# Kernel optimization log

Measured on AMD Instinct MI355X. Metric: run time of the kernel, lower is better.

## Reference

```python
import jax, jax.numpy as jnp
import numpy as np

H = 1024      # hidden_size
NH = 16       # num_attention_heads
HD = H // NH  # attention_head_size = 64
B, S = 2, 2048


def setup_inputs() -> dict:
    key = jax.random.key(0)
    ks = jax.random.split(key, 8)
    scale = 1.0 / np.sqrt(H)
    return {
        "hidden_states": jax.random.normal(ks[0], (B, S, H), dtype=jnp.float32),
        "attention_mask": jnp.zeros((B, 1, 1, S), dtype=jnp.float32),
        "Wq": jax.random.normal(ks[1], (H, H), dtype=jnp.float32) * scale,
        "bq": jax.random.normal(ks[2], (H,), dtype=jnp.float32) * 0.02,
        "Wk": jax.random.normal(ks[3], (H, H), dtype=jnp.float32) * scale,
        "bk": jax.random.normal(ks[4], (H,), dtype=jnp.float32) * 0.02,
        "Wv": jax.random.normal(ks[5], (H, H), dtype=jnp.float32) * scale,
        "bv": jax.random.normal(ks[6], (H,), dtype=jnp.float32) * 0.02,
    }


def _split_heads(x):
    # [B,S,H] -> [B,NH,S,HD]
    b, s, _ = x.shape
    return x.reshape(b, s, NH, HD).transpose(0, 2, 1, 3)


def reference(hidden_states, attention_mask, Wq, bq, Wk, bk, Wv, bv):
    q = _split_heads(hidden_states @ Wq.T + bq)  # [B,NH,S,HD]
    k = _split_heads(hidden_states @ Wk.T + bk)
    v = _split_heads(hidden_states @ Wv.T + bv)
    scores = jnp.einsum("bhqd,bhkd->bhqk", q, k) / np.sqrt(HD).astype(np.float32)
    scores = scores + attention_mask  # additive mask, broadcast over heads/queries
    weights = jax.nn.softmax(scores, axis=-1)  # dropout is identity in eval mode
    ctx = jnp.einsum("bhqk,bhkd->bhqd", weights, v)  # [B,NH,S,HD]
    return ctx.transpose(0, 2, 1, 3).reshape(hidden_states.shape[0], hidden_states.shape[1], H)
```

## Files before the change

kernel.cpp:

```cpp
#include <hip/hip_runtime.h>
#include <hip/hip_bf16.h>
#include <math.h>

#define HSZ   1024
#define NHEAD 16
#define HDIM  64
#define BATCH 2
#define SEQ   2048

#define LOG2E 1.4426950408889634f

typedef __attribute__((ext_vector_type(8))) short short8;
typedef __attribute__((ext_vector_type(4))) short short4_t;
typedef __attribute__((ext_vector_type(4))) float floatx4;

typedef __attribute__((address_space(1))) const unsigned int gu32;
typedef __attribute__((address_space(3))) unsigned int lu32;

__device__ __forceinline__ void g2lds16(const void* g, void* l) {
    __builtin_amdgcn_global_load_lds((gu32*)g, (lu32*)l, 16, 0, 0);
}

__device__ __forceinline__ short f2bf(float f) {
    union { float f; unsigned u; } v; v.f = f;
    unsigned r = (v.u + 0x7FFF + ((v.u >> 16) & 1)) >> 16;
    return (short)r;
}

__device__ __forceinline__ unsigned pk2(float a, float b) {
    __hip_bfloat162 h = __float22bfloat162_rn(make_float2(a, b));
    return *(unsigned*)&h;
}

__device__ __forceinline__ float ex2(float x) {
#if __has_builtin(__builtin_amdgcn_exp2f)
    return __builtin_amdgcn_exp2f(x);
#else
    return exp2f(x);
#endif
}

__global__ __launch_bounds__(256) void convert_kernel(
    const float4* __restrict__ X, const float4* __restrict__ Wq,
    const float4* __restrict__ Wk, const float4* __restrict__ Wv,
    const float4* __restrict__ Mask,
    short4_t* __restrict__ Xb, short4_t* __restrict__ Wb,
    float4* __restrict__ Mw)
{
    int idx = blockIdx.x * 256 + threadIdx.x;
    if (idx >= 1835008) {
        int t = idx - 1835008;
        float4 f = Mask[t];
        float4 o;
        o.x = f.x * LOG2E; o.y = f.y * LOG2E;
        o.z = f.z * LOG2E; o.w = f.w * LOG2E;
        Mw[t] = o;
        return;
    }
    const float4* src; short4_t* dst;
    if (idx < 1048576) { src = X + idx; dst = Xb + idx; }
    else {
        int t = idx - 1048576;
        int sel = t >> 18;
        int wi  = t & 0x3FFFF;
        src = (sel == 0 ? Wq : sel == 1 ? Wk : Wv) + wi;
        dst = Wb + (sel << 18) + wi;
    }
    float4 f = *src;
    short4_t o;
    o.x = f2bf(f.x); o.y = f2bf(f.y); o.z = f2bf(f.z); o.w = f2bf(f.w);
    *dst = o;
}

__global__ __launch_bounds__(256, 3) void qkv_mfma_kernel(
    const short* __restrict__ Xb, const short* __restrict__ Wb,
    const float* __restrict__ bq, const float* __restrict__ bk,
    const float* __restrict__ bv,
    short* __restrict__ qo, short* __restrict__ ko, short* __restrict__ vT)
{
    __shared__ short Sm[128 * 132];
    short* As = Sm;
    short* Bs = Sm + 8192;

    const int tid  = threadIdx.x;
    const int lane = tid & 63;
    const int w    = tid >> 6;
    const int l    = lane & 15, quad = lane >> 4;
    const int gM   = blockIdx.y * 128;
    const int gN   = blockIdx.x * 128;
    const int wm   = (w >> 1) * 64, wn = (w & 1) * 64;
    const int ci   = lane >> 3, pb = lane & 7;

    floatx4 acc[4][4] = {};

    for (int kt = 0; kt < HSZ / 64; ++kt) {
        const int k0 = kt * 64;
        __syncthreads();
        #pragma unroll
        for (int u = 0; u < 4; ++u) {
            int c  = w * 4 + u;
            int r  = c * 8 + ci;
            int lb = pb ^ (r & 7);
            g2lds16(Xb + (size_t)(gM + r) * HSZ + k0 + lb * 8, &As[c * 512]);
            g2lds16(Wb + (size_t)(gN + r) * HSZ + k0 + lb * 8, &Bs[c * 512]);
        }
        __syncthreads();
        #pragma unroll
        for (int kk = 0; kk < 2; ++kk) {
            short8 a[4], b[4];
            #pragma unroll
            for (int i = 0; i < 4; ++i) {
                int m = wm + i * 16 + l;
                a[i] = *(const short8*)&As[m * 64 + (((quad + kk * 4) ^ (m & 7)) << 3)];
                int n = wn + i * 16 + l;
                b[i] = *(const short8*)&Bs[n * 64 + (((quad + kk * 4) ^ (n & 7)) << 3)];
            }
            #pragma unroll
            for (int i = 0; i < 4; ++i)
                #pragma unroll
                for (int j = 0; j < 4; ++j)
                    acc[i][j] = __builtin_amdgcn_mfma_f32_16x16x32_bf16(
                        a[i], b[j], acc[i][j], 0, 0, 0);
        }
    }

    const int mat = gN >> 10;

    if (mat == 2) {
        __syncthreads();
        #pragma unroll
        for (int j = 0; j < 4; ++j) {
            int fl = wn + j * 16 + l;
            float bv_ = bv[(gN & 1023) + fl];
            #pragma unroll
            for (int i = 0; i < 4; ++i)
                #pragma unroll
                for (int r = 0; r < 4; ++r)
                    Sm[fl * 132 + wm + i * 16 + quad * 4 + r]
                        = f2bf(acc[i][j][r] + bv_);
        }
        __syncthreads();
        const int bb = gM >> 11, ss0 = gM & (SEQ - 1);
        #pragma unroll
        for (int it = 0; it < 16; ++it) {
            int f = (tid >> 5) + it * 8;
            int c = (tid & 31) * 4;
            short4_t val = *(const short4_t*)&Sm[f * 132 + c];
            int b = (c >> 2) & 15;
            int cp = (c & ~63) | ((((b & 8) | ((b & 3) << 1) | ((b >> 2) & 1))) << 2);
            int nft = (gN & 1023) + f;
            int head = nft >> 6, d = nft & 63;
            *(short4_t*)&vT[(((size_t)(bb * NHEAD + head)) * HDIM + d) * SEQ
                            + ss0 + cp] = val;
        }
        return;
    }

    const float* bias = (mat == 0) ? bq : bk;
    short* dst        = (mat == 0) ? qo : ko;
    const float qscale = (mat == 0) ? 0.125f * LOG2E : 1.0f;

    #pragma unroll
    for (int j = 0; j < 4; ++j) {
        int nft = (gN & 1023) + wn + j * 16 + l;
        float bv_ = bias[nft];
        int head = nft >> 6, d = nft & 63;
        #pragma unroll
        for (int i = 0; i < 4; ++i) {
            #pragma unroll
            for (int r = 0; r < 4; ++r) {
                int gr = gM + wm + i * 16 + quad * 4 + r;
                int bb = gr >> 11, ss = gr & (SEQ - 1);
                float val = (acc[i][j][r] + bv_) * qscale;
                dst[((((size_t)bb * NHEAD + head) * SEQ + ss) << 6) + d] = f2bf(val);
            }
        }
    }
}

__global__ __launch_bounds__(512, 4) void attn_kernel(
    const short* __restrict__ Qg, const short* __restrict__ Kg,
    const short* __restrict__ VTg, const float* __restrict__ maskw,
    float* __restrict__ out)
{
    __shared__ short Qs[128 * 64];
    __shared__ alignas(16) short Kb3[3][64 * 64];
    __shared__ alignas(16) short Vb3[3][64 * 64];
    __shared__ alignas(16) float Mf[SEQ];

    const int tid  = threadIdx.x;
    const int lane = tid & 63;
    const int w    = tid >> 6;
    const int l    = lane & 15, quad = lane >> 4;
    const int idx  = blockIdx.x;
    const int bh   = idx & 31;
    const int qt   = idx >> 5;
    const int batch = bh >> 4, head = bh & 15;
    const int ci = lane >> 3, pb = lane & 7;

    const short* Qb = Qg + ((size_t)bh * SEQ + qt * 128) * HDIM;
    const short* Kg_ = Kg + (size_t)bh * SEQ * HDIM;
    const short* Vg_ = VTg + (size_t)bh * HDIM * SEQ;
    const float* mrow = maskw + (size_t)batch * SEQ;

    #pragma unroll
    for (int u = 0; u < 2; ++u) {
        int c = w * 2 + u;
        int r = c * 8 + ci;
        int lb = pb ^ (r & 7);
        g2lds16(Qb + (size_t)r * HDIM + lb * 8, &Qs[c * 512]);
    }
    g2lds16(mrow + w * 256 + lane * 4, &Mf[w * 256]);
    {
        int r = w * 8 + ci;
        int lb = pb ^ (r & 7);
        g2lds16(Kg_ + (size_t)r * HDIM + lb * 8,          &Kb3[0][w * 512]);
        g2lds16(Kg_ + (size_t)(64 + r) * HDIM + lb * 8,   &Kb3[1][w * 512]);
        g2lds16(Kg_ + (size_t)(128 + r) * HDIM + lb * 8,  &Kb3[2][w * 512]);
        g2lds16(Vg_ + (size_t)r * SEQ + lb * 8,           &Vb3[0][w * 512]);
        g2lds16(Vg_ + (size_t)r * SEQ + 64 + lb * 8,      &Vb3[1][w * 512]);
    }
    __syncthreads();

    short8 aq[2];
    #pragma unroll
    for (int kk = 0; kk < 2; ++kk) {
        int m = w * 16 + l;
        aq[kk] = *(const short8*)&Qs[m * 64 + (((quad + kk * 4) ^ (m & 7)) << 3)];
    }

    const short8 bones = {(short)0x3F80, (short)0x3F80, (short)0x3F80, (short)0x3F80,
                          (short)0x3F80, (short)0x3F80, (short)0x3F80, (short)0x3F80};

    floatx4 o[4] = {};
    floatx4 ol = {0.f, 0.f, 0.f, 0.f};
    floatx4 sA[4], sB[4];

    const short* kR; const short* kP; short* kW;
    const short* vR; const short* vP; short* vW;

    auto DMAK = [&](int t) {
        int r = w * 8 + ci;
        int lb = pb ^ (r & 7);
        g2lds16(Kg_ + (size_t)(t * 64 + r) * HDIM + lb * 8, kW + w * 512);
    };
    auto DMAV = [&](int t) {
        int r = w * 8 + ci;
        int lb = pb ^ (r & 7);
        g2lds16(Vg_ + (size_t)r * SEQ + t * 64 + lb * 8, vW + w * 512);
    };
    auto ROT = [&]() {
        const short* tk = kR; kR = kP; kP = kW; kW = (short*)tk;
        const short* tv = vR; vR = vP; vP = vW; vW = (short*)tv;
    };

    auto QKT = [&](floatx4 (&s)[4], const short* kbuf, int u1) {
        const float* mg = &Mf[u1 * 64];
        #pragma unroll
        for (int m = 0; m < 4; ++m) {
            float4 mq = *(const float4*)&mg[m * 16 + quad * 4];
            floatx4 ini = {mq.x, mq.y, mq.z, mq.w};
            s[m] = ini;
        }
        #pragma unroll
        for (int kk = 0; kk < 2; ++kk) {
            short8 ak[4];
            #pragma unroll
            for (int m = 0; m < 4; ++m) {
                int kr = m * 16 + l;
                ak[m] = *(const short8*)&kbuf[kr * 64 + (((quad + kk * 4) ^ (kr & 7)) << 3)];
            }
            __builtin_amdgcn_s_setprio(1);
            #pragma unroll
            for (int m = 0; m < 4; ++m)
                s[m] = __builtin_amdgcn_mfma_f32_16x16x32_bf16(
                    ak[m], aq[kk], s[m], 0, 0, 0);
            __builtin_amdgcn_s_setprio(0);
        }
    };

    auto SMPV = [&](floatx4 (&s)[4], const short* vbuf) {
        #pragma unroll
        for (int m = 0; m < 4; ++m) {
            s[m][0] = ex2(s[m][0]);
            s[m][1] = ex2(s[m][1]);
            s[m][2] = ex2(s[m][2]);
            s[m][3] = ex2(s[m][3]);
        }
        #pragma unroll
        for (int kb = 0; kb < 2; ++kb) {
            short8 bvf[4];
            #pragma unroll
            for (int nd = 0; nd < 4; ++nd) {
                int d = nd * 16 + l;
                bvf[nd] = *(const short8*)&vbuf[d * 64 + (((kb * 4 + quad) ^ (d & 7)) << 3)];
            }
            short8 ap;
            {
                union { unsigned u[4]; short8 s8; } pu;
                pu.u[0] = pk2(s[2 * kb][0], s[2 * kb][1]);
                pu.u[1] = pk2(s[2 * kb][2], s[2 * kb][3]);
                pu.u[2] = pk2(s[2 * kb + 1][0], s[2 * kb + 1][1]);
                pu.u[3] = pk2(s[2 * kb + 1][2], s[2 * kb + 1][3]);
                ap = pu.s8;
            }
            __builtin_amdgcn_s_setprio(1);
            #pragma unroll
            for (int nd = 0; nd < 4; ++nd)
                o[nd] = __builtin_amdgcn_mfma_f32_16x16x32_bf16(
                    ap, bvf[nd], o[nd], 0, 0, 0);
            ol = __builtin_amdgcn_mfma_f32_16x16x32_bf16(
                ap, bones, ol, 0, 0, 0);
            __builtin_amdgcn_s_setprio(0);
        }
    };

    QKT(sA, &Kb3[0][0], 0);
    __syncthreads();
    kR = &Kb3[1][0]; kP = &Kb3[2][0]; kW = &Kb3[0][0];
    vR = &Vb3[0][0]; vP = &Vb3[1][0]; vW = &Vb3[2][0];

#define PHASE_BAR(N)                                        \
    asm volatile("s_waitcnt vmcnt(" #N ")" ::: "memory");   \
    __builtin_amdgcn_s_barrier();                           \
    asm volatile("" ::: "memory");

    for (int t = 0; t < 28; t += 2) {
        DMAK(t + 3); DMAV(t + 2);
        QKT(sB, kR, t + 1);
        SMPV(sA, vR);
        PHASE_BAR(2)
        ROT();
        DMAK(t + 4); DMAV(t + 3);
        QKT(sA, kR, t + 2);
        SMPV(sB, vR);
        PHASE_BAR(2)
        ROT();
    }
    DMAK(31); DMAV(30);
    QKT(sB, kR, 29);
    SMPV(sA, vR);
    PHASE_BAR(2)
    ROT();
    DMAV(31);
    QKT(sA, kR, 30);
    SMPV(sB, vR);
    PHASE_BAR(1)
    ROT();
    QKT(sB, kR, 31);
    SMPV(sA, vR);
    PHASE_BAR(0)
    ROT();
    SMPV(sB, vR);
#undef PHASE_BAR

    #pragma unroll
    for (int r = 0; r < 4; ++r) {
        float inv = 1.0f / ol[r];
        int qrow = qt * 128 + w * 16 + quad * 4 + r;
        #pragma unroll
        for (int nd = 0; nd < 4; ++nd)
            out[((size_t)batch * SEQ + qrow) * HSZ + head * HDIM + nd * 16 + l]
                = o[nd][r] * inv;
    }
}

extern "C" void kernel_launch(void* const* d_in, const int* in_sizes, int n_in,
                              void* d_out, int out_size, void* d_ws, size_t ws_size,
                              hipStream_t stream) {
    const float* hs   = (const float*)d_in[0];
    const float* mask = (const float*)d_in[1];
    const float* Wq   = (const float*)d_in[2];
    const float* bq   = (const float*)d_in[3];
    const float* Wk   = (const float*)d_in[4];
    const float* bk   = (const float*)d_in[5];
    const float* Wv   = (const float*)d_in[6];
    const float* bv   = (const float*)d_in[7];
    float* out = (float*)d_out;

    short* Xb = (short*)d_ws;
    short* Wb = Xb + 4194304;
    short* qb = Wb + 3145728;
    short* kb = qb + 4194304;
    short* vT = kb + 4194304;
    float* Mw = (float*)(vT + 4194304);

    convert_kernel<<<7172, 256, 0, stream>>>(
        (const float4*)hs, (const float4*)Wq, (const float4*)Wk, (const float4*)Wv,
        (const float4*)mask, (short4_t*)Xb, (short4_t*)Wb, (float4*)Mw);

    dim3 g2(3 * HSZ / 128, BATCH * SEQ / 128);
    qkv_mfma_kernel<<<g2, 256, 0, stream>>>(Xb, Wb, bq, bk, bv, qb, kb, vT);

    attn_kernel<<<512, 512, 0, stream>>>(qb, kb, vT, Mw, out);
}
```

Measured before the change: 156.5 us.

## Load Q fragments directly from global and fold mask scaling into attention

Drops the Q staging buffer in LDS and loads each wave's Q MFMA fragments straight from global memory into registers. Removes the mask pre-scaling pass from the convert kernel and instead multiplies the raw mask by log2(e) when initializing score accumulators. This frees 16KB of LDS per block, which may allow more resident blocks, and removes a small extra write and read of the scaled mask. In exchange the Q reads are less coalesced, and a few extra multiplies land in the inner loop.

```diff
diff --git a/kernel.cpp b/kernel.cpp
--- a/kernel.cpp
+++ b/kernel.cpp
@@ -43,20 +43,9 @@
 __global__ __launch_bounds__(256) void convert_kernel(
     const float4* __restrict__ X, const float4* __restrict__ Wq,
     const float4* __restrict__ Wk, const float4* __restrict__ Wv,
-    const float4* __restrict__ Mask,
-    short4_t* __restrict__ Xb, short4_t* __restrict__ Wb,
-    float4* __restrict__ Mw)
+    short4_t* __restrict__ Xb, short4_t* __restrict__ Wb)
 {
     int idx = blockIdx.x * 256 + threadIdx.x;
-    if (idx >= 1835008) {
-        int t = idx - 1835008;
-        float4 f = Mask[t];
-        float4 o;
-        o.x = f.x * LOG2E; o.y = f.y * LOG2E;
-        o.z = f.z * LOG2E; o.w = f.w * LOG2E;
-        Mw[t] = o;
-        return;
-    }
     const float4* src; short4_t* dst;
     if (idx < 1048576) { src = X + idx; dst = Xb + idx; }
     else {
@@ -183,7 +172,6 @@
     const short* __restrict__ VTg, const float* __restrict__ maskw,
     float* __restrict__ out)
 {
-    __shared__ short Qs[128 * 64];
     __shared__ alignas(16) short Kb3[3][64 * 64];
     __shared__ alignas(16) short Vb3[3][64 * 64];
     __shared__ alignas(16) float Mf[SEQ];
@@ -203,13 +191,6 @@
     const short* Vg_ = VTg + (size_t)bh * HDIM * SEQ;
     const float* mrow = maskw + (size_t)batch * SEQ;
 
-    #pragma unroll
-    for (int u = 0; u < 2; ++u) {
-        int c = w * 2 + u;
-        int r = c * 8 + ci;
-        int lb = pb ^ (r & 7);
-        g2lds16(Qb + (size_t)r * HDIM + lb * 8, &Qs[c * 512]);
-    }
     g2lds16(mrow + w * 256 + lane * 4, &Mf[w * 256]);
     {
         int r = w * 8 + ci;
@@ -220,14 +201,13 @@
         g2lds16(Vg_ + (size_t)r * SEQ + lb * 8,           &Vb3[0][w * 512]);
         g2lds16(Vg_ + (size_t)r * SEQ + 64 + lb * 8,      &Vb3[1][w * 512]);
     }
-    __syncthreads();
 
     short8 aq[2];
     #pragma unroll
-    for (int kk = 0; kk < 2; ++kk) {
-        int m = w * 16 + l;
-        aq[kk] = *(const short8*)&Qs[m * 64 + (((quad + kk * 4) ^ (m & 7)) << 3)];
-    }
+    for (int kk = 0; kk < 2; ++kk)
+        aq[kk] = *(const short8*)&Qb[(w * 16 + l) * HDIM + kk * 32 + quad * 8];
+
+    __syncthreads();
 
     const short8 bones = {(short)0x3F80, (short)0x3F80, (short)0x3F80, (short)0x3F80,
                           (short)0x3F80, (short)0x3F80, (short)0x3F80, (short)0x3F80};
@@ -259,7 +239,8 @@
         #pragma unroll
         for (int m = 0; m < 4; ++m) {
             float4 mq = *(const float4*)&mg[m * 16 + quad * 4];
-            floatx4 ini = {mq.x, mq.y, mq.z, mq.w};
+            floatx4 ini = {mq.x * LOG2E, mq.y * LOG2E,
+                           mq.z * LOG2E, mq.w * LOG2E};
             s[m] = ini;
         }
         #pragma unroll
@@ -383,14 +364,13 @@
     short* qb = Wb + 3145728;
     short* kb = qb + 4194304;
     short* vT = kb + 4194304;
-    float* Mw = (float*)(vT + 4194304);
-
-    convert_kernel<<<7172, 256, 0, stream>>>(
+
+    convert_kernel<<<7168, 256, 0, stream>>>(
         (const float4*)hs, (const float4*)Wq, (const float4*)Wk, (const float4*)Wv,
-        (const float4*)mask, (short4_t*)Xb, (short4_t*)Wb, (float4*)Mw);
+        (short4_t*)Xb, (short4_t*)Wb);
 
     dim3 g2(3 * HSZ / 128, BATCH * SEQ / 128);
     qkv_mfma_kernel<<<g2, 256, 0, stream>>>(Xb, Wb, bq, bk, bv, qb, kb, vT);
 
-    attn_kernel<<<512, 512, 0, stream>>>(qb, kb, vT, Mw, out);
-}
+    attn_kernel<<<512, 512, 0, stream>>>(qb, kb, vT, mask, out);
+}
```

Measured after the change: 158.5 us. About the same (+1.3%).

## Rework QKV GEMM into 256x256 tiles with double-buffered async LDS pipeline

Applied to the files above, without the earlier changes.

The QKV projection GEMM now uses 256x256 output tiles per 512-thread block, giving 192 blocks instead of 768. K-tiles are double-buffered in LDS, and the next tile's global-to-LDS loads are interleaved with the four MFMA phases, using explicit barriers and s_setprio around the MFMA bursts. The intent is to hide global load latency and raise data reuse per block, at the cost of more LDS and registers per block. The V transpose epilogue is split into two halves so it fits the reused LDS buffer.

```diff
diff --git a/kernel.cpp b/kernel.cpp
--- a/kernel.cpp
+++ b/kernel.cpp
@@ -72,86 +72,118 @@
     *dst = o;
 }
 
-__global__ __launch_bounds__(256, 3) void qkv_mfma_kernel(
+__global__ __launch_bounds__(512, 2) void qkv_mfma_kernel(
     const short* __restrict__ Xb, const short* __restrict__ Wb,
     const float* __restrict__ bq, const float* __restrict__ bk,
     const float* __restrict__ bv,
     short* __restrict__ qo, short* __restrict__ ko, short* __restrict__ vT)
 {
-    __shared__ short Sm[128 * 132];
-    short* As = Sm;
-    short* Bs = Sm + 8192;
+    __shared__ alignas(16) short As[2][2][128 * 64];
+    __shared__ alignas(16) short Bs[2][2][128 * 64];
 
     const int tid  = threadIdx.x;
     const int lane = tid & 63;
     const int w    = tid >> 6;
     const int l    = lane & 15, quad = lane >> 4;
-    const int gM   = blockIdx.y * 128;
-    const int gN   = blockIdx.x * 128;
-    const int wm   = (w >> 1) * 64, wn = (w & 1) * 64;
+    const int wr   = w >> 2, wc = w & 3;
     const int ci   = lane >> 3, pb = lane & 7;
-
-    floatx4 acc[4][4] = {};
-
-    for (int kt = 0; kt < HSZ / 64; ++kt) {
-        const int k0 = kt * 64;
-        __syncthreads();
-        #pragma unroll
-        for (int u = 0; u < 4; ++u) {
-            int c  = w * 4 + u;
+    const int bid  = blockIdx.x;
+    const int gM   = (bid / 12) * 256;
+    const int gN   = (bid % 12) * 256;
+
+    auto STAGE = [&](int t, int db, int op , int half) {
+        #pragma unroll
+        for (int u = 0; u < 2; ++u) {
+            int c  = w * 2 + u;
             int r  = c * 8 + ci;
             int lb = pb ^ (r & 7);
-            g2lds16(Xb + (size_t)(gM + r) * HSZ + k0 + lb * 8, &As[c * 512]);
-            g2lds16(Wb + (size_t)(gN + r) * HSZ + k0 + lb * 8, &Bs[c * 512]);
-        }
-        __syncthreads();
-        #pragma unroll
-        for (int kk = 0; kk < 2; ++kk) {
+            const short* src = (op == 0)
+                ? Xb + (size_t)(gM + half * 128 + r) * HSZ + t * 64 + lb * 8
+                : Wb + (size_t)(gN + half * 128 + r) * HSZ + t * 64 + lb * 8;
+            short* dst = (op == 0 ? &As[db][half][0] : &Bs[db][half][0]) + c * 512;
+            g2lds16(src, dst);
+        }
+    };
+
+    floatx4 acc[8][4] = {};
+
+    STAGE(0, 0, 0, 0); STAGE(0, 0, 0, 1);
+    STAGE(0, 0, 1, 0); STAGE(0, 0, 1, 1);
+    asm volatile("s_waitcnt vmcnt(0)" ::: "memory");
+    __builtin_amdgcn_s_barrier();
+
+    for (int t = 0; t < HSZ / 64; ++t) {
+        const int d = t & 1, dn = d ^ 1;
+        const short* Ah = &As[d][wr][0];
+        const short* Bh = &Bs[d][wc >> 1][0];
+        const int bbase = (wc & 1) * 64;
+        const bool more = (t + 1 < HSZ / 64);
+        #pragma unroll
+        for (int ph = 0; ph < 4; ++ph) {
+            const int mh = ph & 1, kkv = ph >> 1;
             short8 a[4], b[4];
             #pragma unroll
             for (int i = 0; i < 4; ++i) {
-                int m = wm + i * 16 + l;
-                a[i] = *(const short8*)&As[m * 64 + (((quad + kk * 4) ^ (m & 7)) << 3)];
-                int n = wn + i * 16 + l;
-                b[i] = *(const short8*)&Bs[n * 64 + (((quad + kk * 4) ^ (n & 7)) << 3)];
-            }
+                int lr = (mh * 4 + i) * 16 + l;
+                a[i] = *(const short8*)&Ah[lr * 64 + (((quad + kkv * 4) ^ (lr & 7)) << 3)];
+                int br = bbase + i * 16 + l;
+                b[i] = *(const short8*)&Bh[br * 64 + (((quad + kkv * 4) ^ (br & 7)) << 3)];
+            }
+            if (more) {
+                if      (ph == 0) STAGE(t + 1, dn, 0, 0);
+                else if (ph == 1) STAGE(t + 1, dn, 1, 0);
+                else if (ph == 2) STAGE(t + 1, dn, 1, 1);
+                else              STAGE(t + 1, dn, 0, 1);
+            }
+            __builtin_amdgcn_s_barrier();
+            asm volatile("s_waitcnt lgkmcnt(0)" ::: "memory");
+            __builtin_amdgcn_s_setprio(1);
             #pragma unroll
             for (int i = 0; i < 4; ++i)
                 #pragma unroll
                 for (int j = 0; j < 4; ++j)
-                    acc[i][j] = __builtin_amdgcn_mfma_f32_16x16x32_bf16(
-                        a[i], b[j], acc[i][j], 0, 0, 0);
+                    acc[mh * 4 + i][j] = __builtin_amdgcn_mfma_f32_16x16x32_bf16(
+                        a[i], b[j], acc[mh * 4 + i][j], 0, 0, 0);
+            __builtin_amdgcn_s_setprio(0);
+            if (ph == 3) asm volatile("s_waitcnt vmcnt(0)" ::: "memory");
+            __builtin_amdgcn_s_barrier();
         }
     }
 
     const int mat = gN >> 10;
 
     if (mat == 2) {
-        __syncthreads();
-        #pragma unroll
-        for (int j = 0; j < 4; ++j) {
-            int fl = wn + j * 16 + l;
-            float bv_ = bv[(gN & 1023) + fl];
-            #pragma unroll
-            for (int i = 0; i < 4; ++i)
+        short* Smv = &As[0][0][0];
+        const int bb = gM >> 11, ss0 = gM & (SEQ - 1);
+        #pragma unroll
+        for (int h = 0; h < 2; ++h) {
+            __syncthreads();
+            if ((wc >> 1) == h) {
                 #pragma unroll
-                for (int r = 0; r < 4; ++r)
-                    Sm[fl * 132 + wm + i * 16 + quad * 4 + r]
-                        = f2bf(acc[i][j][r] + bv_);
-        }
-        __syncthreads();
-        const int bb = gM >> 11, ss0 = gM & (SEQ - 1);
-        #pragma unroll
-        for (int it = 0; it < 16; ++it) {
-            int f = (tid >> 5) + it * 8;
-            int c = (tid & 31) * 4;
-            short4_t val = *(const short4_t*)&Sm[f * 132 + c];
-            int b = (c >> 2) & 15;
-            int cp = (c & ~63) | ((((b & 8) | ((b & 3) << 1) | ((b >> 2) & 1))) << 2);
-            int nft = (gN & 1023) + f;
-            int head = nft >> 6, d = nft & 63;
-            *(short4_t*)&vT[(((size_t)(bb * NHEAD + head)) * HDIM + d) * SEQ
-                            + ss0 + cp] = val;
+                for (int j = 0; j < 4; ++j) {
+                    int fl = (wc & 1) * 64 + j * 16 + l;
+                    float bv_ = bv[(gN & 1023) + h * 128 + fl];
+                    #pragma unroll
+                    for (int i = 0; i < 8; ++i)
+                        #pragma unroll
+                        for (int r = 0; r < 4; ++r)
+                            Smv[fl * 260 + wr * 128 + i * 16 + quad * 4 + r]
+                                = f2bf(acc[i][j][r] + bv_);
+                }
+            }
+            __syncthreads();
+            #pragma unroll
+            for (int it = 0; it < 16; ++it) {
+                int f = (tid >> 6) + it * 8;
+                int c = (tid & 63) * 4;
+                short4_t val = *(const short4_t*)&Smv[f * 260 + c];
+                int b = (c >> 2) & 15;
+                int cp = (c & ~63) | ((((b & 8) | ((b & 3) << 1) | ((b >> 2) & 1))) << 2);
+                int nft = (gN & 1023) + h * 128 + f;
+                int head = nft >> 6, d = nft & 63;
+                *(short4_t*)&vT[(((size_t)(bb * NHEAD + head)) * HDIM + d) * SEQ
+                                + ss0 + cp] = val;
+            }
         }
         return;
     }
@@ -162,17 +194,17 @@
 
     #pragma unroll
     for (int j = 0; j < 4; ++j) {
-        int nft = (gN & 1023) + wn + j * 16 + l;
+        int nft = (gN & 1023) + wc * 64 + j * 16 + l;
         float bv_ = bias[nft];
         int head = nft >> 6, d = nft & 63;
         #pragma unroll
-        for (int i = 0; i < 4; ++i) {
+        for (int i = 0; i < 8; ++i) {
             #pragma unroll
             for (int r = 0; r < 4; ++r) {
-                int gr = gM + wm + i * 16 + quad * 4 + r;
-                int bb = gr >> 11, ss = gr & (SEQ - 1);
+                int gr = gM + wr * 128 + i * 16 + quad * 4 + r;
+                int bb2 = gr >> 11, ss = gr & (SEQ - 1);
                 float val = (acc[i][j][r] + bv_) * qscale;
-                dst[((((size_t)bb * NHEAD + head) * SEQ + ss) << 6) + d] = f2bf(val);
+                dst[((((size_t)bb2 * NHEAD + head) * SEQ + ss) << 6) + d] = f2bf(val);
             }
         }
     }
@@ -389,8 +421,7 @@
         (const float4*)hs, (const float4*)Wq, (const float4*)Wk, (const float4*)Wv,
         (const float4*)mask, (short4_t*)Xb, (short4_t*)Wb, (float4*)Mw);
 
-    dim3 g2(3 * HSZ / 128, BATCH * SEQ / 128);
-    qkv_mfma_kernel<<<g2, 256, 0, stream>>>(Xb, Wb, bq, bk, bv, qb, kb, vT);
+    qkv_mfma_kernel<<<192, 512, 0, stream>>>(Xb, Wb, bq, bk, bv, qb, kb, vT);
 
     attn_kernel<<<512, 512, 0, stream>>>(qb, kb, vT, Mw, out);
 }
```

Result: slower. 171.4 us (+9.5%).
